# Optimization experiments

Measured on AMD Instinct MI355X. Metric: run time of the kernel, lower is better.

The kernel has to match this reference:

```python
import jax, jax.numpy as jnp
import numpy as np


def setup_inputs() -> dict:
    key = jax.random.key(0)
    k1, k2 = jax.random.split(key)
    B, T, N = 4, 8, 2048
    pred = jax.random.normal(k1, (B, T, N), dtype=jnp.float32)
    target = jax.random.normal(k2, (B, T, N), dtype=jnp.float32)
    return {"pred": pred, "target": target}


def reference(pred, target):
    # Kendall-tau loss: sort target by pred order, count concordant/discordant pairs.
    pred = pred.astype(jnp.float32)
    target = target.astype(jnp.float32)
    idx = jnp.argsort(pred, axis=2)                      # [B,T,N]
    target_a = jnp.take_along_axis(target, idx, axis=2)  # [B,T,N]
    B, T, N = target_a.shape
    M = N - 1
    refs = target_a[:, :, :-1, None]                     # [B,T,M,1] (row i = i-th element)
    ex = target_a[:, :, None, :]                         # [B,T,1,N] (col j = j-th element)
    mask = jnp.triu(jnp.ones((M, N), dtype=bool), k=1)   # pairs with j > i
    greater = (ex > refs) & mask                         # [B,T,M,N]
    lesser = (ex < refs) & mask
    conc = jnp.sum(greater, axis=(-1, -2))[..., None].astype(jnp.float32)  # [B,T,1]
    disc = jnp.sum(lesser, axis=(-1, -2))[..., None].astype(jnp.float32)
    tau = (conc - disc) / (conc + disc)
    loss = 1.0 - tau
    return loss.mean()
```

## Files before the change

### kernel.cpp

```cpp
#include <hip/hip_runtime.h>

#define NN 2048
#define ROWS 32
#define TJ 64
#define JT (NN / TJ)
#define IB 8
#define THREADS 256
#define GRID (ROWS * JT)

static_assert(JT == 32, "block decode uses &31 / >>5");
static_assert(THREADS * IB == NN, "block must cover full i range");

typedef float v2f __attribute__((ext_vector_type(2)));

__global__ __launch_bounds__(THREADS) void ktau_count(const float* __restrict__ pred,
                                                      const float* __restrict__ target,
                                                      int* __restrict__ ws) {
    __shared__ v2f jtile[TJ];
    __shared__ int wpart[THREADS / 64];

    const int blk = blockIdx.x;
    const int row = blk >> 5;
    const int jt  = blk & (JT - 1);
    const float* __restrict__ prow = pred   + row * NN;
    const float* __restrict__ qrow = target + row * NN;
    const int tid = threadIdx.x;

    if (tid < TJ) {
        int j = jt * TJ + tid;
        v2f v; v.x = prow[j]; v.y = qrow[j];
        jtile[tid] = v;
    }

    v2f pq[IB];
    {
        const float4* p4 = (const float4*)(prow + tid * IB);
        const float4* q4 = (const float4*)(qrow + tid * IB);
        float4 a0 = p4[0], a1 = p4[1];
        float4 b0 = q4[0], b1 = q4[1];
        pq[0].x=a0.x; pq[0].y=b0.x;  pq[1].x=a0.y; pq[1].y=b0.y;
        pq[2].x=a0.z; pq[2].y=b0.z;  pq[3].x=a0.w; pq[3].y=b0.w;
        pq[4].x=a1.x; pq[4].y=b1.x;  pq[5].x=a1.y; pq[5].y=b1.y;
        pq[6].x=a1.z; pq[6].y=b1.z;  pq[7].x=a1.w; pq[7].y=b1.w;
    }
    __syncthreads();

    unsigned acc[4] = {0u, 0u, 0u, 0u};
    #pragma unroll 8
    for (int jj = 0; jj < TJ; ++jj) {
        v2f pqj = jtile[jj];
        #pragma unroll
        for (int k = 0; k < IB; ++k) {
            v2f d = pqj - pq[k];
            int x = (__float_as_int(d.x) ^ __float_as_int(d.y));
            acc[k & 3] += ((unsigned)x) >> 31;
        }
    }
    int disc = (int)(acc[0] + acc[1] + acc[2] + acc[3]);

    #pragma unroll
    for (int off = 32; off > 0; off >>= 1)
        disc += __shfl_down(disc, off, 64);
    if ((tid & 63) == 0)
        wpart[tid >> 6] = disc;
    __syncthreads();
    if (tid == 0)
        ws[blk] = wpart[0] + wpart[1] + wpart[2] + wpart[3];
}

__global__ __launch_bounds__(256) void ktau_final(const int* __restrict__ ws,
                                                  float* __restrict__ out) {
    __shared__ int wpart[4];
    const int tid = threadIdx.x;
    int v = 0;
    #pragma unroll
    for (int b = tid; b < GRID; b += 256) v += ws[b];
    #pragma unroll
    for (int off = 32; off > 0; off >>= 1)
        v += __shfl_down(v, off, 64);
    if ((tid & 63) == 0) wpart[tid >> 6] = v;
    __syncthreads();
    if (tid == 0) {
        const float invT = 1.0f / (float)(((long long)NN * (NN - 1)) / 2);
        int total = wpart[0] + wpart[1] + wpart[2] + wpart[3];
        out[0] = (float)total * invT / (float)ROWS;
    }
}

extern "C" void kernel_launch(void* const* d_in, const int* in_sizes, int n_in,
                              void* d_out, int out_size, void* d_ws, size_t ws_size,
                              hipStream_t stream) {
    const float* pred   = (const float*)d_in[0];
    const float* target = (const float*)d_in[1];
    float* out = (float*)d_out;
    int* ws    = (int*)d_ws;

    ktau_count<<<GRID, THREADS, 0, stream>>>(pred, target, ws);
    ktau_final<<<1, 256, 0, stream>>>(ws, out);
}
```

Before: 69.37 us.

## Exploit pair symmetry with triangular tile pairs and bit-packed popcount counting

The grid now covers only the upper-triangular tile pairs of the 2048x2048 pair matrix, using 128-wide tiles and 64-thread blocks. Off-diagonal counts are doubled because the sign-discordance test is symmetric, which removes roughly half of the pairwise comparisons. The per-pair add is replaced by funnel-shifting the sign bits into a 32-bit word with alignbit and popcounting it afterwards, which lowers ALU work per comparison. The cost is a serial loop to decode the tile pair, many more small blocks, and less parallelism per block.

```diff
diff --git a/kernel.cpp b/kernel.cpp
--- a/kernel.cpp
+++ b/kernel.cpp
@@ -2,70 +2,66 @@
 
 #define NN 2048
 #define ROWS 32
-#define TJ 64
-#define JT (NN / TJ)
-#define IB 8
-#define THREADS 256
-#define GRID (ROWS * JT)
-
-static_assert(JT == 32, "block decode uses &31 / >>5");
-static_assert(THREADS * IB == NN, "block must cover full i range");
+#define TS 128
+#define NT (NN / TS)
+#define NPAIR (NT * (NT + 1) / 2)
+#define GRID (ROWS * NPAIR)
+#define THREADS 64
 
 typedef float v2f __attribute__((ext_vector_type(2)));
 
 __global__ __launch_bounds__(THREADS) void ktau_count(const float* __restrict__ pred,
                                                       const float* __restrict__ target,
                                                       int* __restrict__ ws) {
-    __shared__ v2f jtile[TJ];
-    __shared__ int wpart[THREADS / 64];
+    __shared__ v2f jtile[TS];
 
     const int blk = blockIdx.x;
-    const int row = blk >> 5;
-    const int jt  = blk & (JT - 1);
+    const int row = blk / NPAIR;
+    int t = blk - row * NPAIR;
+    int ta = 0, base = 0;
+    while (t >= base + (NT - ta)) { base += NT - ta; ++ta; }
+    const int tb = ta + (t - base);
+
     const float* __restrict__ prow = pred   + row * NN;
     const float* __restrict__ qrow = target + row * NN;
     const int tid = threadIdx.x;
 
-    if (tid < TJ) {
-        int j = jt * TJ + tid;
+    #pragma unroll
+    for (int t2 = tid; t2 < TS; t2 += THREADS) {
+        int j = tb * TS + t2;
         v2f v; v.x = prow[j]; v.y = qrow[j];
-        jtile[tid] = v;
+        jtile[t2] = v;
     }
 
-    v2f pq[IB];
-    {
-        const float4* p4 = (const float4*)(prow + tid * IB);
-        const float4* q4 = (const float4*)(qrow + tid * IB);
-        float4 a0 = p4[0], a1 = p4[1];
-        float4 b0 = q4[0], b1 = q4[1];
-        pq[0].x=a0.x; pq[0].y=b0.x;  pq[1].x=a0.y; pq[1].y=b0.y;
-        pq[2].x=a0.z; pq[2].y=b0.z;  pq[3].x=a0.w; pq[3].y=b0.w;
-        pq[4].x=a1.x; pq[4].y=b1.x;  pq[5].x=a1.y; pq[5].y=b1.y;
-        pq[6].x=a1.z; pq[6].y=b1.z;  pq[7].x=a1.w; pq[7].y=b1.w;
-    }
+    const int i0 = ta * TS + tid * 2;
+    float2 pp = *(const float2*)(prow + i0);
+    float2 qq = *(const float2*)(qrow + i0);
+    v2f pq0; pq0.x = pp.x; pq0.y = qq.x;
+    v2f pq1; pq1.x = pp.y; pq1.y = qq.y;
     __syncthreads();
 
-    unsigned acc[4] = {0u, 0u, 0u, 0u};
-    #pragma unroll 8
-    for (int jj = 0; jj < TJ; ++jj) {
-        v2f pqj = jtile[jj];
+    unsigned disc = 0;
+    for (int h = 0; h < TS / 32; ++h) {
+        unsigned b0 = 0, b1 = 0;
         #pragma unroll
-        for (int k = 0; k < IB; ++k) {
-            v2f d = pqj - pq[k];
-            int x = (__float_as_int(d.x) ^ __float_as_int(d.y));
-            acc[k & 3] += ((unsigned)x) >> 31;
+        for (int jj = 0; jj < 32; ++jj) {
+            v2f pqj = jtile[h * 32 + jj];
+            v2f d0 = pqj - pq0;
+            v2f d1 = pqj - pq1;
+            unsigned x0 = (unsigned)(__float_as_int(d0.x) ^ __float_as_int(d0.y));
+            unsigned x1 = (unsigned)(__float_as_int(d1.x) ^ __float_as_int(d1.y));
+            b0 = __builtin_amdgcn_alignbit(b0, x0, 31);
+            b1 = __builtin_amdgcn_alignbit(b1, x1, 31);
         }
+        disc += __builtin_popcount(b0) + __builtin_popcount(b1);
     }
-    int disc = (int)(acc[0] + acc[1] + acc[2] + acc[3]);
 
+    int d = (int)disc;
     #pragma unroll
     for (int off = 32; off > 0; off >>= 1)
-        disc += __shfl_down(disc, off, 64);
-    if ((tid & 63) == 0)
-        wpart[tid >> 6] = disc;
-    __syncthreads();
+        d += __shfl_down(d, off, 64);
     if (tid == 0)
-        ws[blk] = wpart[0] + wpart[1] + wpart[2] + wpart[3];
+        ws[blk] = (ta == tb) ? d : (d << 1);
 }
 
 __global__ __launch_bounds__(256) void ktau_final(const int* __restrict__ ws,
@@ -73,7 +69,6 @@
     __shared__ int wpart[4];
     const int tid = threadIdx.x;
     int v = 0;
-    #pragma unroll
     for (int b = tid; b < GRID; b += 256) v += ws[b];
     #pragma unroll
     for (int off = 32; off > 0; off >>= 1)
```

Result: faster. 67.72 us, median of 2 (-2.4%).
